# Performance work log

Hardware: AMD Instinct MI355X
Metric: run time of the kernel (lower is better)

## Reference

```python
import jax, jax.numpy as jnp
import numpy as np

H, W = 16, 16
DIM = 512
HEADS = 8
DIM_HEAD = 64
INNER = HEADS * DIM_HEAD  # 512
B = 8
N = H * W  # 256
SCALE = DIM_HEAD ** -0.5
EPS = 1e-5


def _index_map(h, w):
    # index_map[n, m] = dx * (2w-1) + dy with dx = x-i+h-1, dy = y-j+w-1
    xs = np.arange(h)
    ys = np.arange(w)
    dx = xs[:, None] - xs[None, :] + h - 1            # (h, h)
    dy = ys[:, None] - ys[None, :] + w - 1            # (w, w)
    idx = dx[:, None, :, None] * (2 * w - 1) + dy[None, :, None, :]  # (h, w, h, w)
    return idx.reshape(h * w, h * w).astype(np.int32)


def setup_inputs() -> dict:
    key = jax.random.key(0)
    ks = jax.random.split(key, 5)
    x = jax.random.normal(ks[0], (B, N, DIM), dtype=jnp.float32)
    ln_g = jnp.ones((DIM,), jnp.float32)
    ln_b = jnp.zeros((DIM,), jnp.float32)
    w_qkv = jax.random.normal(ks[1], (DIM, 3 * INNER), jnp.float32) * 0.02
    unique_params = jax.random.normal(ks[2], ((2 * H - 1) * (2 * W - 1), INNER), jnp.float32) * 0.02
    w_out = jax.random.normal(ks[3], (INNER, DIM), jnp.float32) * 0.02
    b_out = jnp.zeros((DIM,), jnp.float32)
    idx_map = jnp.asarray(_index_map(H, W))  # (N, N) int32
    return {"x": x, "ln_g": ln_g, "ln_b": ln_b, "w_qkv": w_qkv,
            "unique_params": unique_params, "w_out": w_out, "b_out": b_out,
            "idx_map": idx_map}


def reference(x, ln_g, ln_b, w_qkv, unique_params, w_out, b_out, idx_map):
    b, n, _ = x.shape
    # LayerNorm
    mu = jnp.mean(x, axis=-1, keepdims=True)
    var = jnp.mean(jnp.square(x - mu), axis=-1, keepdims=True)
    xn = (x - mu) * jax.lax.rsqrt(var + EPS) * ln_g + ln_b
    # qkv projection (no bias)
    qkv = xn @ w_qkv                                  # (b, n, 3*inner)
    q, k, v = jnp.split(qkv, 3, axis=-1)
    q = q.reshape(b, n, HEADS, DIM_HEAD)
    k = k.reshape(b, n, HEADS, DIM_HEAD)
    v = v.reshape(b, n, HEADS, DIM_HEAD)
    # attention scores
    dots = jnp.einsum('bnhd,bmhd->bhnm', q, k) * SCALE
    attn = jax.nn.softmax(dots, axis=-1)              # (b, h, n, m)
    # relative-position table: (n, m, h, d)
    rpos = unique_params[idx_map].reshape(n, n, HEADS, DIM_HEAD)
    # out[b,h,n,d] = sum_m attn[b,h,n,m] * (v[b,m,h,d] + rpos[n,m,h,d])
    out = jnp.einsum('bhnm,bmhd->bnhd', attn, v) \
        + jnp.einsum('bhnm,nmhd->bnhd', attn, rpos)
    out = out.reshape(b, n, INNER)
    return out @ w_out + b_out
```

## Files before the change

kernel.cpp:

```cpp
#include <hip/hip_runtime.h>
#include <math.h>

#define NB 8
#define SEQ 256
#define DIMC 512
#define NHEAD 8
#define DHEAD 64
#define SCALEF 0.125f

typedef __attribute__((ext_vector_type(8))) short s16x8;
typedef __attribute__((ext_vector_type(4))) float f32x4;

typedef __attribute__((address_space(3))) unsigned int lds_u32_t;
typedef const __attribute__((address_space(1))) unsigned int g_u32_t;
static __device__ __forceinline__ void gl_lds16(const void* gsrc, void* ldst) {
  __builtin_amdgcn_global_load_lds((g_u32_t*)gsrc, (lds_u32_t*)ldst, 16, 0, 0);
}

static __device__ __forceinline__ unsigned short f2bf(float f) {
  union { float f; unsigned u; } c; c.f = f;
  unsigned r = c.u + 0x7FFF + ((c.u >> 16) & 1);
  return (unsigned short)(r >> 16);
}
static __device__ __forceinline__ float bf2f(unsigned short u) {
  union { unsigned u; float f; } c; c.u = ((unsigned)u) << 16;
  return c.f;
}

static __device__ void tcast_body(const float* __restrict__ W,
    unsigned short* __restrict__ WT, int K, int N, int n0, int k0, int t,
    float (*tile)[65]) {
#pragma unroll
  for (int i = 0; i < 16; ++i) {
    const int idx = i * 256 + t;
    const int kl = idx >> 6, nl = idx & 63;
    tile[kl][nl] = W[(size_t)(k0 + kl) * N + n0 + nl];
  }
  __syncthreads();
#pragma unroll
  for (int i = 0; i < 16; ++i) {
    const int idx = i * 256 + t;
    const int nl = idx >> 6, kl = idx & 63;
    WT[(size_t)(n0 + nl) * K + k0 + kl] = f2bf(tile[kl][nl]);
  }
}

__global__ __launch_bounds__(256) void prep_kernel(const float* __restrict__ x,
    const float* __restrict__ g, const float* __restrict__ bta,
    const float* __restrict__ w_qkv, const float* __restrict__ w_out,
    const float* __restrict__ up, unsigned short* __restrict__ xnb,
    unsigned short* __restrict__ wqt, unsigned short* __restrict__ wot,
    unsigned short* __restrict__ upb) {
  __shared__ float tile[64][65];
  __shared__ float sh_s[4], sh_q[4];
  const int t = threadIdx.x;
  const int bid = blockIdx.x;
  if (bid < 192) {
    tcast_body(w_qkv, wqt, 512, 1536, (bid % 24) * 64, (bid / 24) * 64, t, tile);
  } else if (bid < 256) {
    const int b2 = bid - 192;
    tcast_body(w_out, wot, 512, 512, (b2 % 8) * 64, (b2 / 8) * 64, t, tile);
  } else if (bid < 497) {
    const int base = (bid - 256) * 2048 + t * 4;
#pragma unroll
    for (int it = 0; it < 2; ++it) {
      const int i = base + it * 1024;
      if (i < 492032) {
        const float4 v = *(const float4*)&up[i];
        ushort4 w;
        w.x = f2bf(v.x); w.y = f2bf(v.y); w.z = f2bf(v.z); w.w = f2bf(v.w);
        *(ushort4*)&upb[i] = w;
      }
    }
  } else {
    const int row = bid - 497;
    const float2 v = ((const float2*)(x + (size_t)row * DIMC))[t];
    float s = v.x + v.y;
    float q = v.x * v.x + v.y * v.y;
#pragma unroll
    for (int off = 32; off > 0; off >>= 1) {
      s += __shfl_down(s, off);
      q += __shfl_down(q, off);
    }
    const int wave = t >> 6, lane = t & 63;
    if (lane == 0) { sh_s[wave] = s; sh_q[wave] = q; }
    __syncthreads();
    const float fs = sh_s[0] + sh_s[1] + sh_s[2] + sh_s[3];
    const float fq = sh_q[0] + sh_q[1] + sh_q[2] + sh_q[3];
    const float mean = fs * (1.0f / DIMC);
    const float inv = rsqrtf(fq * (1.0f / DIMC) - mean * mean + 1e-5f);
    const float2 gv = ((const float2*)g)[t];
    const float2 bv = ((const float2*)bta)[t];
    ushort2 o;
    o.x = f2bf((v.x - mean) * inv * gv.x + bv.x);
    o.y = f2bf((v.y - mean) * inv * gv.y + bv.y);
    ((ushort2*)(xnb + (size_t)row * DIMC))[t] = o;
  }
}

template <int BM, int BN, bool BIAS, bool OUTBF>
__global__ __launch_bounds__(256) void mfma_gemm_bt(
    const unsigned short* __restrict__ A, const unsigned short* __restrict__ BT,
    const float* __restrict__ bias, void* __restrict__ Cv,
    int M, int K, int N) {
  constexpr int TR = BM / 32;
  constexpr int TC = BN / 32;
  __shared__ unsigned short As[BM * 32];
  __shared__ unsigned short Bs[BN * 32];
  const int t = threadIdx.x;
  const int wave = t >> 6, lane = t & 63;
  const int wr = wave >> 1, wc = wave & 1;
  const int bm = blockIdx.x * BM, bn = blockIdx.y * BN;

  f32x4 acc[TR][TC] = {};

  const int fr = lane & 15, q4 = lane >> 4;
  const int kBlocks = K >> 5;
  for (int kb = 0; kb < kBlocks; ++kb) {
    const int k0 = kb << 5;
    __syncthreads();
#pragma unroll
    for (int c = 0; c < BM * 4 / 256; ++c) {
      const int p = c * 256 + t;
      const int row = p >> 2;
      const int jl = (p & 3) ^ ((row >> 1) & 3);
      gl_lds16(A + (size_t)(bm + row) * K + k0 + jl * 8,
               As + (size_t)(c * 256 + wave * 64) * 8);
    }
#pragma unroll
    for (int c = 0; c < BN * 4 / 256; ++c) {
      const int p = c * 256 + t;
      const int row = p >> 2;
      const int jl = (p & 3) ^ ((row >> 1) & 3);
      gl_lds16(BT + (size_t)(bn + row) * K + k0 + jl * 8,
               Bs + (size_t)(c * 256 + wave * 64) * 8);
    }
    __syncthreads();
    s16x8 af[TR], bfr[TC];
#pragma unroll
    for (int i = 0; i < TR; ++i) {
      const int row = wr * (BM / 2) + i * 16 + fr;
      const int jp = q4 ^ ((row >> 1) & 3);
      af[i] = *(const s16x8*)(As + row * 32 + jp * 8);
    }
#pragma unroll
    for (int j = 0; j < TC; ++j) {
      const int row = wc * (BN / 2) + j * 16 + fr;
      const int jp = q4 ^ ((row >> 1) & 3);
      bfr[j] = *(const s16x8*)(Bs + row * 32 + jp * 8);
    }
#pragma unroll
    for (int i = 0; i < TR; ++i)
#pragma unroll
      for (int j = 0; j < TC; ++j)
        acc[i][j] = __builtin_amdgcn_mfma_f32_16x16x32_bf16(af[i], bfr[j],
                                                            acc[i][j], 0, 0, 0);
  }
#pragma unroll
  for (int i = 0; i < TR; ++i) {
#pragma unroll
    for (int j = 0; j < TC; ++j) {
      const int col = bn + wc * (BN / 2) + j * 16 + fr;
      const float bv = BIAS ? bias[col] : 0.0f;
#pragma unroll
      for (int r = 0; r < 4; ++r) {
        const int row = bm + wr * (BM / 2) + i * 16 + q4 * 4 + r;
        if constexpr (OUTBF) {
          ((unsigned short*)Cv)[(size_t)row * N + col] = f2bf(acc[i][j][r] + bv);
        } else {
          ((float*)Cv)[(size_t)row * N + col] = acc[i][j][r] + bv;
        }
      }
    }
  }
}

#define PSTR 264
#define KSTR 72
__global__ __launch_bounds__(256) void fused_attn_kernel(
    const unsigned short* __restrict__ qkvb, unsigned short* __restrict__ attnb,
    unsigned short* __restrict__ oav) {
  __shared__ unsigned short kv_lds[256 * KSTR];
  __shared__ unsigned short p_lds[64 * PSTR];
  const int bh = blockIdx.y, b = bh >> 3, h = bh & 7;
  const int n0 = blockIdx.x * 64;
  const int t = threadIdx.x, wave = t >> 6, lane = t & 63;
  const int fr = lane & 15, q4 = lane >> 4;

  {
    const int dc = (t & 7) * 8;
#pragma unroll
    for (int p = 0; p < 8; ++p) {
      const int m = p * 32 + (t >> 3);
      const s16x8 v =
          *(const s16x8*)(qkvb + (size_t)(b * SEQ + m) * 1536 + 512 + h * 64 + dc);
      *(s16x8*)(kv_lds + m * KSTR + dc) = v;
    }
  }
  s16x8 qf[2];
  {
    const size_t qrow = (size_t)(b * SEQ + n0 + wave * 16 + fr) * 1536 + h * 64;
#pragma unroll
    for (int ks = 0; ks < 2; ++ks)
      qf[ks] = *(const s16x8*)(qkvb + qrow + ks * 32 + q4 * 8);
  }
  __syncthreads();

  f32x4 s[16];
#pragma unroll
  for (int mt = 0; mt < 16; ++mt) s[mt] = (f32x4){0.f, 0.f, 0.f, 0.f};
#pragma unroll
  for (int ks = 0; ks < 2; ++ks)
#pragma unroll
    for (int mt = 0; mt < 16; ++mt) {
      const s16x8 kf =
          *(const s16x8*)(kv_lds + (mt * 16 + fr) * KSTR + ks * 32 + q4 * 8);
      s[mt] = __builtin_amdgcn_mfma_f32_16x16x32_bf16(qf[ks], kf, s[mt], 0, 0, 0);
    }

  float mx[4] = {-1e30f, -1e30f, -1e30f, -1e30f};
#pragma unroll
  for (int mt = 0; mt < 16; ++mt)
#pragma unroll
    for (int r = 0; r < 4; ++r) {
      s[mt][r] *= SCALEF;
      mx[r] = fmaxf(mx[r], s[mt][r]);
    }
#pragma unroll
  for (int r = 0; r < 4; ++r) {
    mx[r] = fmaxf(mx[r], __shfl_xor(mx[r], 1));
    mx[r] = fmaxf(mx[r], __shfl_xor(mx[r], 2));
    mx[r] = fmaxf(mx[r], __shfl_xor(mx[r], 4));
    mx[r] = fmaxf(mx[r], __shfl_xor(mx[r], 8));
  }
  float sum[4] = {0.f, 0.f, 0.f, 0.f};
#pragma unroll
  for (int mt = 0; mt < 16; ++mt)
#pragma unroll
    for (int r = 0; r < 4; ++r) {
      s[mt][r] = __expf(s[mt][r] - mx[r]);
      sum[r] += s[mt][r];
    }
#pragma unroll
  for (int r = 0; r < 4; ++r) {
    sum[r] += __shfl_xor(sum[r], 1);
    sum[r] += __shfl_xor(sum[r], 2);
    sum[r] += __shfl_xor(sum[r], 4);
    sum[r] += __shfl_xor(sum[r], 8);
  }
  const float invs[4] = {1.0f / sum[0], 1.0f / sum[1], 1.0f / sum[2],
                         1.0f / sum[3]};

  __syncthreads();

  {
    const int nb = wave * 16 + q4 * 4;
#pragma unroll
    for (int mt = 0; mt < 16; ++mt)
#pragma unroll
      for (int r = 0; r < 4; ++r)
        p_lds[(nb + r) * PSTR + mt * 16 + fr] = f2bf(s[mt][r] * invs[r]);
  }
  {
    const int dc = (t & 7) * 8;
#pragma unroll
    for (int p = 0; p < 8; ++p) {
      const int m = p * 32 + (t >> 3);
      const s16x8 v =
          *(const s16x8*)(qkvb + (size_t)(b * SEQ + m) * 1536 + 1024 + h * 64 + dc);
#pragma unroll
      for (int j = 0; j < 8; ++j) kv_lds[(dc + j) * PSTR + m] = v[j];
    }
  }
  __syncthreads();

#pragma unroll
  for (int p = 0; p < 8; ++p) {
    const int idx = p * 256 + t;
    const int row = idx >> 5, mc = (idx & 31) * 8;
    *(s16x8*)(attnb + (size_t)(bh * SEQ + n0 + row) * SEQ + mc) =
        *(const s16x8*)(p_lds + row * PSTR + mc);
  }

  f32x4 o[4];
#pragma unroll
  for (int dt = 0; dt < 4; ++dt) o[dt] = (f32x4){0.f, 0.f, 0.f, 0.f};
#pragma unroll
  for (int ks = 0; ks < 8; ++ks) {
    const s16x8 pf =
        *(const s16x8*)(p_lds + (wave * 16 + fr) * PSTR + ks * 32 + q4 * 8);
#pragma unroll
    for (int dt = 0; dt < 4; ++dt) {
      const s16x8 vf =
          *(const s16x8*)(kv_lds + (dt * 16 + fr) * PSTR + ks * 32 + q4 * 8);
      o[dt] = __builtin_amdgcn_mfma_f32_16x16x32_bf16(pf, vf, o[dt], 0, 0, 0);
    }
  }
#pragma unroll
  for (int dt = 0; dt < 4; ++dt)
#pragma unroll
    for (int r = 0; r < 4; ++r) {
      const int n = n0 + wave * 16 + q4 * 4 + r;
      oav[(size_t)(b * SEQ + n) * DIMC + h * 64 + dt * 16 + fr] = f2bf(o[dt][r]);
    }
}

#define RSTRIDE 280
__global__ __launch_bounds__(256) void rpos_kernel(
    const unsigned short* __restrict__ attnb, const unsigned short* __restrict__ upb,
    unsigned short* __restrict__ ob) {
  __shared__ float aS[4][8 * RSTRIDE];
  const int t = threadIdx.x;
  const int wave = t >> 6, lane = t & 63;
  const int g = lane >> 4, dg = lane & 15;
  const int pair = blockIdx.x * 4 + wave;
  const int n = pair >> 3, h = pair & 7;
  float* aW = aS[wave];

  const int m4 = lane * 4;
  const int sm4 = m4 + ((m4 >> 6) << 3);
#pragma unroll
  for (int b = 0; b < 8; ++b) {
    const ushort4 v =
        *(const ushort4*)&attnb[(size_t)((b * 8 + h) * SEQ + n) * SEQ + m4];
    float4 f;
    f.x = bf2f(v.x); f.y = bf2f(v.y); f.z = bf2f(v.z); f.w = bf2f(v.w);
    *(float4*)&aW[b * RSTRIDE + sm4] = f;
  }
  __syncthreads();

  const int xn = n >> 4, yn = n & 15;
  float acc[8][4];
#pragma unroll
  for (int b = 0; b < 8; ++b)
#pragma unroll
    for (int j = 0; j < 4; ++j) acc[b][j] = 0.0f;

  const int mbase = g * 64;
  const int sbase = g * 72;
#pragma unroll 4
  for (int mm = 0; mm < 64; ++mm) {
    const int m = mbase + mm;
    const int xm = m >> 4, ym = m & 15;
    const int row = (xn - xm + 15) * 31 + (yn - ym + 15);
    const ushort4 uu = *(const ushort4*)&upb[(size_t)row * DIMC + h * 64 + dg * 4];
    const float ux = bf2f(uu.x), uy = bf2f(uu.y), uz = bf2f(uu.z), uw = bf2f(uu.w);
    float ab[8];
#pragma unroll
    for (int b = 0; b < 8; ++b) ab[b] = aW[b * RSTRIDE + sbase + mm];
#pragma unroll
    for (int b = 0; b < 8; ++b) {
      acc[b][0] += ab[b] * ux;
      acc[b][1] += ab[b] * uy;
      acc[b][2] += ab[b] * uz;
      acc[b][3] += ab[b] * uw;
    }
  }
#pragma unroll
  for (int b = 0; b < 8; ++b)
#pragma unroll
    for (int j = 0; j < 4; ++j) {
      float v = acc[b][j];
      v += __shfl_xor(v, 16);
      v += __shfl_xor(v, 32);
      acc[b][j] = v;
    }
#pragma unroll
  for (int k = 0; k < 2; ++k) {
    const int b = g * 2 + k;
    const size_t base = (size_t)(b * SEQ + n) * DIMC + h * 64 + dg * 4;
    ushort4 pv = *(ushort4*)&ob[base];
    ushort4 w;
    w.x = f2bf(bf2f(pv.x) + acc[b][0]);
    w.y = f2bf(bf2f(pv.y) + acc[b][1]);
    w.z = f2bf(bf2f(pv.z) + acc[b][2]);
    w.w = f2bf(bf2f(pv.w) + acc[b][3]);
    *(ushort4*)&ob[base] = w;
  }
}

extern "C" void kernel_launch(void* const* d_in, const int* in_sizes, int n_in,
                              void* d_out, int out_size, void* d_ws,
                              size_t ws_size, hipStream_t stream) {
  const float* x = (const float*)d_in[0];
  const float* ln_g = (const float*)d_in[1];
  const float* ln_b = (const float*)d_in[2];
  const float* w_qkv = (const float*)d_in[3];
  const float* up = (const float*)d_in[4];
  const float* w_out = (const float*)d_in[5];
  const float* b_out = (const float*)d_in[6];
  float* out = (float*)d_out;

  unsigned short* u = (unsigned short*)d_ws;
  unsigned short* qkvb = u;
  unsigned short* attnb = u + 3145728;
  unsigned short* xnb = u + 7340032;
  unsigned short* ob = u + 8388608;
  unsigned short* wqt = u + 9437184;
  unsigned short* wot = u + 10223616;
  unsigned short* upb = u + 10485760;
  if (ws_size < (size_t)10977792 * sizeof(unsigned short)) return;

  prep_kernel<<<2545, 256, 0, stream>>>(x, ln_g, ln_b, w_qkv, w_out, up,
                                        xnb, wqt, wot, upb);
  mfma_gemm_bt<128, 128, false, true>
      <<<dim3(16, 12), 256, 0, stream>>>(xnb, wqt, nullptr, qkvb, 2048, 512, 1536);
  fused_attn_kernel<<<dim3(4, 64), 256, 0, stream>>>(qkvb, attnb, ob);
  rpos_kernel<<<512, 256, 0, stream>>>(attnb, upb, ob);
  mfma_gemm_bt<64, 64, true, false>
      <<<dim3(32, 8), 256, 0, stream>>>(ob, wot, b_out, out, 2048, 512, 512);
}
```

Measured before the change: 123.2 us.

## Emit transposed V from QKV GEMM and shrink tiles for more blocks

The QKV GEMM epilogue now writes the V columns directly in a per-head transposed layout (b,h,d,m), so the attention kernel loads V^T with vectorized reads instead of scattering scalar transposes into LDS. The attention kernel is halved to 128 threads and 32 query rows per block. The rpos kernel now splits the batch across two waves, and both GEMMs use smaller tiles. Together these raise block counts and occupancy on the many CUs, at the cost of more redundant K/V loads and strided scalar stores of V^T in the GEMM epilogue.

```diff
diff --git a/kernel.cpp b/kernel.cpp
--- a/kernel.cpp
+++ b/kernel.cpp
@@ -98,11 +98,11 @@
   }
 }
 
-template <int BM, int BN, bool BIAS, bool OUTBF>
+template <int BM, int BN, bool BIAS, bool OUTBF, bool VSPLIT>
 __global__ __launch_bounds__(256) void mfma_gemm_bt(
     const unsigned short* __restrict__ A, const unsigned short* __restrict__ BT,
     const float* __restrict__ bias, void* __restrict__ Cv,
-    int M, int K, int N) {
+    unsigned short* __restrict__ vtb, int M, int K, int N) {
   constexpr int TR = BM / 32;
   constexpr int TC = BN / 32;
   __shared__ unsigned short As[BM * 32];
@@ -120,20 +120,24 @@
     const int k0 = kb << 5;
     __syncthreads();
 #pragma unroll
-    for (int c = 0; c < BM * 4 / 256; ++c) {
+    for (int c = 0; c < (BM * 4 + 255) / 256; ++c) {
       const int p = c * 256 + t;
-      const int row = p >> 2;
-      const int jl = (p & 3) ^ ((row >> 1) & 3);
-      gl_lds16(A + (size_t)(bm + row) * K + k0 + jl * 8,
-               As + (size_t)(c * 256 + wave * 64) * 8);
-    }
-#pragma unroll
-    for (int c = 0; c < BN * 4 / 256; ++c) {
+      if (BM * 4 % 256 == 0 || p < BM * 4) {
+        const int row = p >> 2;
+        const int jl = (p & 3) ^ ((row >> 1) & 3);
+        gl_lds16(A + (size_t)(bm + row) * K + k0 + jl * 8,
+                 As + (size_t)(c * 256 + wave * 64) * 8);
+      }
+    }
+#pragma unroll
+    for (int c = 0; c < (BN * 4 + 255) / 256; ++c) {
       const int p = c * 256 + t;
-      const int row = p >> 2;
-      const int jl = (p & 3) ^ ((row >> 1) & 3);
-      gl_lds16(BT + (size_t)(bn + row) * K + k0 + jl * 8,
-               Bs + (size_t)(c * 256 + wave * 64) * 8);
+      if (BN * 4 % 256 == 0 || p < BN * 4) {
+        const int row = p >> 2;
+        const int jl = (p & 3) ^ ((row >> 1) & 3);
+        gl_lds16(BT + (size_t)(bn + row) * K + k0 + jl * 8,
+                 Bs + (size_t)(c * 256 + wave * 64) * 8);
+      }
     }
     __syncthreads();
     s16x8 af[TR], bfr[TC];
@@ -155,6 +159,23 @@
       for (int j = 0; j < TC; ++j)
         acc[i][j] = __builtin_amdgcn_mfma_f32_16x16x32_bf16(af[i], bfr[j],
                                                             acc[i][j], 0, 0, 0);
+  }
+  if (VSPLIT && bn >= 1024) {
+#pragma unroll
+    for (int i = 0; i < TR; ++i) {
+#pragma unroll
+      for (int j = 0; j < TC; ++j) {
+        const int hc = bn - 1024 + wc * (BN / 2) + j * 16 + fr;
+        const int h = hc >> 6, d = hc & 63;
+#pragma unroll
+        for (int r = 0; r < 4; ++r) {
+          const int row = bm + wr * (BM / 2) + i * 16 + q4 * 4 + r;
+          const int b = row >> 8, m = row & 255;
+          vtb[(size_t)((b * 8 + h) * 64 + d) * 256 + m] = f2bf(acc[i][j][r]);
+        }
+      }
+    }
+    return;
   }
 #pragma unroll
   for (int i = 0; i < TR; ++i) {
@@ -177,25 +198,22 @@
 
 #define PSTR 264
 #define KSTR 72
-__global__ __launch_bounds__(256) void fused_attn_kernel(
-    const unsigned short* __restrict__ qkvb, unsigned short* __restrict__ attnb,
-    unsigned short* __restrict__ oav) {
+__global__ __launch_bounds__(128) void fused_attn_kernel(
+    const unsigned short* __restrict__ qkvb, const unsigned short* __restrict__ vtb,
+    unsigned short* __restrict__ attnb, unsigned short* __restrict__ oav) {
   __shared__ unsigned short kv_lds[256 * KSTR];
-  __shared__ unsigned short p_lds[64 * PSTR];
+  __shared__ unsigned short p_lds[32 * PSTR];
   const int bh = blockIdx.y, b = bh >> 3, h = bh & 7;
-  const int n0 = blockIdx.x * 64;
+  const int n0 = blockIdx.x * 32;
   const int t = threadIdx.x, wave = t >> 6, lane = t & 63;
   const int fr = lane & 15, q4 = lane >> 4;
 
-  {
-    const int dc = (t & 7) * 8;
-#pragma unroll
-    for (int p = 0; p < 8; ++p) {
-      const int m = p * 32 + (t >> 3);
-      const s16x8 v =
-          *(const s16x8*)(qkvb + (size_t)(b * SEQ + m) * 1536 + 512 + h * 64 + dc);
-      *(s16x8*)(kv_lds + m * KSTR + dc) = v;
-    }
+#pragma unroll
+  for (int p = 0; p < 16; ++p) {
+    const int chunk = p * 128 + t;
+    const int m = chunk >> 3, c = chunk & 7;
+    *(s16x8*)(kv_lds + m * KSTR + c * 8) =
+        *(const s16x8*)(qkvb + (size_t)(b * SEQ + m) * 1536 + 512 + h * 64 + c * 8);
   }
   s16x8 qf[2];
   {
@@ -261,22 +279,18 @@
       for (int r = 0; r < 4; ++r)
         p_lds[(nb + r) * PSTR + mt * 16 + fr] = f2bf(s[mt][r] * invs[r]);
   }
-  {
-    const int dc = (t & 7) * 8;
-#pragma unroll
-    for (int p = 0; p < 8; ++p) {
-      const int m = p * 32 + (t >> 3);
-      const s16x8 v =
-          *(const s16x8*)(qkvb + (size_t)(b * SEQ + m) * 1536 + 1024 + h * 64 + dc);
-#pragma unroll
-      for (int j = 0; j < 8; ++j) kv_lds[(dc + j) * PSTR + m] = v[j];
-    }
+#pragma unroll
+  for (int p = 0; p < 16; ++p) {
+    const int idx = p * 128 + t;
+    const int d = idx >> 5, c = idx & 31;
+    *(s16x8*)(kv_lds + d * PSTR + c * 8) =
+        *(const s16x8*)(vtb + (size_t)(bh * 64 + d) * 256 + c * 8);
   }
   __syncthreads();
 
 #pragma unroll
   for (int p = 0; p < 8; ++p) {
-    const int idx = p * 256 + t;
+    const int idx = p * 128 + t;
     const int row = idx >> 5, mc = (idx & 31) * 8;
     *(s16x8*)(attnb + (size_t)(bh * SEQ + n0 + row) * SEQ + mc) =
         *(const s16x8*)(p_lds + row * PSTR + mc);
@@ -309,32 +323,35 @@
 __global__ __launch_bounds__(256) void rpos_kernel(
     const unsigned short* __restrict__ attnb, const unsigned short* __restrict__ upb,
     unsigned short* __restrict__ ob) {
-  __shared__ float aS[4][8 * RSTRIDE];
+  __shared__ float aS[4][4 * RSTRIDE];
   const int t = threadIdx.x;
   const int wave = t >> 6, lane = t & 63;
   const int g = lane >> 4, dg = lane & 15;
-  const int pair = blockIdx.x * 4 + wave;
-  const int n = pair >> 3, h = pair & 7;
+  const int idx = blockIdx.x * 4 + wave;
+  const int bhalf = idx & 1;
+  const int h = (idx >> 1) & 7;
+  const int n = idx >> 4;
   float* aW = aS[wave];
 
   const int m4 = lane * 4;
   const int sm4 = m4 + ((m4 >> 6) << 3);
 #pragma unroll
-  for (int b = 0; b < 8; ++b) {
+  for (int bl = 0; bl < 4; ++bl) {
+    const int b = bhalf * 4 + bl;
     const ushort4 v =
         *(const ushort4*)&attnb[(size_t)((b * 8 + h) * SEQ + n) * SEQ + m4];
     float4 f;
     f.x = bf2f(v.x); f.y = bf2f(v.y); f.z = bf2f(v.z); f.w = bf2f(v.w);
-    *(float4*)&aW[b * RSTRIDE + sm4] = f;
+    *(float4*)&aW[bl * RSTRIDE + sm4] = f;
   }
   __syncthreads();
 
   const int xn = n >> 4, yn = n & 15;
-  float acc[8][4];
-#pragma unroll
-  for (int b = 0; b < 8; ++b)
-#pragma unroll
-    for (int j = 0; j < 4; ++j) acc[b][j] = 0.0f;
+  float acc[4][4];
+#pragma unroll
+  for (int bl = 0; bl < 4; ++bl)
+#pragma unroll
+    for (int j = 0; j < 4; ++j) acc[bl][j] = 0.0f;
 
   const int mbase = g * 64;
   const int sbase = g * 72;
@@ -345,36 +362,35 @@
     const int row = (xn - xm + 15) * 31 + (yn - ym + 15);
     const ushort4 uu = *(const ushort4*)&upb[(size_t)row * DIMC + h * 64 + dg * 4];
     const float ux = bf2f(uu.x), uy = bf2f(uu.y), uz = bf2f(uu.z), uw = bf2f(uu.w);
-    float ab[8];
-#pragma unroll
-    for (int b = 0; b < 8; ++b) ab[b] = aW[b * RSTRIDE + sbase + mm];
-#pragma unroll
-    for (int b = 0; b < 8; ++b) {
-      acc[b][0] += ab[b] * ux;
-      acc[b][1] += ab[b] * uy;
-      acc[b][2] += ab[b] * uz;
-      acc[b][3] += ab[b] * uw;
-    }
-  }
-#pragma unroll
-  for (int b = 0; b < 8; ++b)
+    float ab[4];
+#pragma unroll
+    for (int bl = 0; bl < 4; ++bl) ab[bl] = aW[bl * RSTRIDE + sbase + mm];
+#pragma unroll
+    for (int bl = 0; bl < 4; ++bl) {
+      acc[bl][0] += ab[bl] * ux;
+      acc[bl][1] += ab[bl] * uy;
+      acc[bl][2] += ab[bl] * uz;
+      acc[bl][3] += ab[bl] * uw;
+    }
+  }
+#pragma unroll
+  for (int bl = 0; bl < 4; ++bl)
 #pragma unroll
     for (int j = 0; j < 4; ++j) {
-      float v = acc[b][j];
+      float v = acc[bl][j];
       v += __shfl_xor(v, 16);
       v += __shfl_xor(v, 32);
-      acc[b][j] = v;
-    }
-#pragma unroll
-  for (int k = 0; k < 2; ++k) {
-    const int b = g * 2 + k;
+      acc[bl][j] = v;
+    }
+  {
+    const int b = bhalf * 4 + g;
     const size_t base = (size_t)(b * SEQ + n) * DIMC + h * 64 + dg * 4;
     ushort4 pv = *(ushort4*)&ob[base];
     ushort4 w;
-    w.x = f2bf(bf2f(pv.x) + acc[b][0]);
-    w.y = f2bf(bf2f(pv.y) + acc[b][1]);
-    w.z = f2bf(bf2f(pv.z) + acc[b][2]);
-    w.w = f2bf(bf2f(pv.w) + acc[b][3]);
+    w.x = f2bf(bf2f(pv.x) + acc[g][0]);
+    w.y = f2bf(bf2f(pv.y) + acc[g][1]);
+    w.z = f2bf(bf2f(pv.z) + acc[g][2]);
+    w.w = f2bf(bf2f(pv.w) + acc[g][3]);
     *(ushort4*)&ob[base] = w;
   }
 }
@@ -399,14 +415,17 @@
   unsigned short* wqt = u + 9437184;
   unsigned short* wot = u + 10223616;
   unsigned short* upb = u + 10485760;
-  if (ws_size < (size_t)10977792 * sizeof(unsigned short)) return;
+  unsigned short* vtb = u + 10977792;
+  if (ws_size < (size_t)12026368 * sizeof(unsigned short)) return;
 
   prep_kernel<<<2545, 256, 0, stream>>>(x, ln_g, ln_b, w_qkv, w_out, up,
                                         xnb, wqt, wot, upb);
-  mfma_gemm_bt<128, 128, false, true>
-      <<<dim3(16, 12), 256, 0, stream>>>(xnb, wqt, nullptr, qkvb, 2048, 512, 1536);
-  fused_attn_kernel<<<dim3(4, 64), 256, 0, stream>>>(qkvb, attnb, ob);
-  rpos_kernel<<<512, 256, 0, stream>>>(attnb, upb, ob);
-  mfma_gemm_bt<64, 64, true, false>
-      <<<dim3(32, 8), 256, 0, stream>>>(ob, wot, b_out, out, 2048, 512, 512);
-}
+  mfma_gemm_bt<64, 64, false, true, true>
+      <<<dim3(32, 24), 256, 0, stream>>>(xnb, wqt, nullptr, qkvb, vtb,
+                                         2048, 512, 1536);
+  fused_attn_kernel<<<dim3(8, 64), 128, 0, stream>>>(qkvb, vtb, attnb, ob);
+  rpos_kernel<<<1024, 256, 0, stream>>>(attnb, upb, ob);
+  mfma_gemm_bt<64, 32, true, false, false>
+      <<<dim3(32, 16), 256, 0, stream>>>(ob, wot, b_out, out, nullptr,
+                                         2048, 512, 512);
+}
```

After: 120.5 us (median of 2 runs). 2.2% less time.
